# Kernel optimization log

Measured on AMD Instinct MI355X. Metric: run time of the kernel, lower is better.

Reference implementation:

```python
import jax, jax.numpy as jnp
import numpy as np

# NF4 codebook (QLoRA): 16 quantile values of a standard normal, normalized to [-1, 1]
NF4_TABLE = jnp.array([
    -1.0, -0.6961928009986877, -0.5250730514526367, -0.39491748809814453,
    -0.28444138169288635, -0.18477343022823334, -0.09105003625154495, 0.0,
    0.07958029955625534, 0.16093020141124725, 0.24611230194568634,
    0.33791524171829224, 0.44070982933044434, 0.5626170039176941,
    0.7229568362236328, 1.0], dtype=jnp.float32)

IN_DIM = 4096
OUT_DIM = 4096
RANK = 16
ALPHA = 32.0
BLOCK = 64  # NF4 quantization block size along the flattened weight


def setup_inputs() -> dict:
    key = jax.random.key(0)
    k1, k2, k3, k4, k5 = jax.random.split(key, 5)
    x = jax.random.normal(k1, (4, 2048, IN_DIM), dtype=jnp.float32)
    # 4-bit codes into NF4_TABLE, stored unpacked as int32
    w_codes = jax.random.randint(k2, (OUT_DIM, IN_DIM), 0, 16, dtype=jnp.int32)
    # per-block absmax scales (positive)
    w_scales = jax.random.uniform(k3, (OUT_DIM, IN_DIM // BLOCK), dtype=jnp.float32) * 0.02 + 1e-3
    # lora_a: kaiming-uniform-ish scale; lora_b: nonzero for testability (original inits to zeros)
    lora_a = jax.random.normal(k4, (RANK, IN_DIM), dtype=jnp.float32) * (1.0 / np.sqrt(IN_DIM))
    lora_b = jax.random.normal(k5, (OUT_DIM, RANK), dtype=jnp.float32) * 0.01
    return {"x": x, "w_codes": w_codes, "w_scales": w_scales, "lora_a": lora_a, "lora_b": lora_b}


def _dequant_nf4(w_codes, w_scales):
    # codes [O, I] -> dequantized weight [O, I]
    w = NF4_TABLE[w_codes]                                   # [O, I]
    w = w.reshape(OUT_DIM, IN_DIM // BLOCK, BLOCK) * w_scales[:, :, None]
    return w.reshape(OUT_DIM, IN_DIM)


def reference(x, w_codes, w_scales, lora_a, lora_b):
    # base: frozen NF4 linear (dequantize then matmul), no bias
    w = _dequant_nf4(w_codes, w_scales)                      # [O, I]
    base = jnp.einsum('bsi,oi->bso', x, w)                   # [B, S, O]
    # LoRA path: dropout p=0.0 -> identity; scale alpha / rank
    ax = jnp.einsum('bsi,ri->bsr', x, lora_a)                # [B, S, r]
    lora = jnp.einsum('bsr,or->bso', ax, lora_b)             # [B, S, O]
    return base + (ALPHA / RANK) * lora
```

## Files before the change

kernel.cpp:

```cpp
#include <hip/hip_runtime.h>
#include <hip/hip_bf16.h>


#define IN_DIM  4096
#define OUT_DIM 4096
#define RANK    16
#define M_TOK   8192
#define LORA_SCALE 2.0f

typedef __bf16 bf16_t;
typedef bf16_t bf16x8 __attribute__((ext_vector_type(8)));
typedef float  f32x4  __attribute__((ext_vector_type(4)));

__device__ __constant__ float NF4_TAB[16] = {
    -1.0f, -0.6961928009986877f, -0.5250730514526367f, -0.39491748809814453f,
    -0.28444138169288635f, -0.18477343022823334f, -0.09105003625154495f, 0.0f,
    0.07958029955625534f, 0.16093020141124725f, 0.24611230194568634f,
    0.33791524171829224f, 0.44070982933044434f, 0.5626170039176941f,
    0.7229568362236328f, 1.0f};

__global__ __launch_bounds__(256) void prep_w(
    const int* __restrict__ codes, const float* __restrict__ scales,
    const float* __restrict__ la, const float* __restrict__ lb,
    bf16_t* __restrict__ W)
{
    __shared__ float nf4s[16];
    __shared__ float lbs[4][16];
    const int o0 = blockIdx.x * 4;
    const int tid = threadIdx.x;
    if (tid < 64) lbs[tid >> 4][tid & 15] = lb[(o0 + (tid >> 4)) * RANK + (tid & 15)] * LORA_SCALE;
    else if (tid < 80) nf4s[tid - 64] = NF4_TAB[tid - 64];
    __syncthreads();

    #pragma unroll
    for (int it = 0; it < 2; ++it) {
        const int i0 = (it * 256 + tid) * 8;
        float w[4][8];
        #pragma unroll
        for (int oo = 0; oo < 4; ++oo) {
            const size_t base = (size_t)(o0 + oo) * IN_DIM + i0;
            int4 c0 = *(const int4*)(codes + base);
            int4 c1 = *(const int4*)(codes + base + 4);
            const float sc = scales[(o0 + oo) * (IN_DIM / 64) + (i0 >> 6)];
            w[oo][0] = nf4s[c0.x] * sc; w[oo][1] = nf4s[c0.y] * sc;
            w[oo][2] = nf4s[c0.z] * sc; w[oo][3] = nf4s[c0.w] * sc;
            w[oo][4] = nf4s[c1.x] * sc; w[oo][5] = nf4s[c1.y] * sc;
            w[oo][6] = nf4s[c1.z] * sc; w[oo][7] = nf4s[c1.w] * sc;
        }
        #pragma unroll
        for (int r = 0; r < RANK; ++r) {
            float4 a0 = *(const float4*)(la + r * IN_DIM + i0);
            float4 a1 = *(const float4*)(la + r * IN_DIM + i0 + 4);
            #pragma unroll
            for (int oo = 0; oo < 4; ++oo) {
                const float b = lbs[oo][r];
                w[oo][0] += b * a0.x; w[oo][1] += b * a0.y;
                w[oo][2] += b * a0.z; w[oo][3] += b * a0.w;
                w[oo][4] += b * a1.x; w[oo][5] += b * a1.y;
                w[oo][6] += b * a1.z; w[oo][7] += b * a1.w;
            }
        }
        #pragma unroll
        for (int oo = 0; oo < 4; ++oo) {
            bf16x8 v;
            #pragma unroll
            for (int j = 0; j < 8; ++j) v[j] = (bf16_t)w[oo][j];
            *(bf16x8*)(W + (size_t)(o0 + oo) * IN_DIM + i0) = v;
        }
    }
}

__global__ __launch_bounds__(256) void cast_x(
    const float* __restrict__ x, bf16_t* __restrict__ y, int n8)
{
    const int stride = gridDim.x * blockDim.x;
    for (int i = blockIdx.x * blockDim.x + threadIdx.x; i < n8; i += stride) {
        const size_t e = (size_t)i * 8;
        float4 a = *(const float4*)(x + e);
        float4 b = *(const float4*)(x + e + 4);
        bf16x8 v;
        v[0] = (bf16_t)a.x; v[1] = (bf16_t)a.y; v[2] = (bf16_t)a.z; v[3] = (bf16_t)a.w;
        v[4] = (bf16_t)b.x; v[5] = (bf16_t)b.y; v[6] = (bf16_t)b.z; v[7] = (bf16_t)b.w;
        *(bf16x8*)(y + e) = v;
    }
}

__global__ __launch_bounds__(512, 2) void gemm_bt(
    const bf16_t* __restrict__ A, const bf16_t* __restrict__ B,
    float* __restrict__ C)
{
    __shared__ __align__(128) char lds[131072];

    const int tid  = threadIdx.x;
    const int wave = tid >> 6;
    const int lane = tid & 63;

    const int flat = blockIdx.y * gridDim.x + blockIdx.x;
    const int swz  = (flat & 7) * 64 + (flat >> 3);
    const int bx = swz & 15;
    const int by = swz >> 4;
    const int m0 = by * 256;
    const int n0 = bx * 256;

    const int wr = wave >> 2;
    const int wc = wave & 3;

    f32x4 acc[8][4];
    #pragma unroll
    for (int i = 0; i < 8; ++i)
        #pragma unroll
        for (int j = 0; j < 4; ++j) acc[i][j] = (f32x4)0.0f;

    const int frow = lane & 15;
    const int fch  = lane >> 4;

    int offA[8], offB0[2], offB1[2];
    #pragma unroll
    for (int f = 0; f < 8; ++f) {
        const int r = wr * 128 + f * 16 + frow;
        offA[f] = r * 64 + ((fch ^ ((r >> 1) & 3)) << 4);
    }
    #pragma unroll
    for (int n = 0; n < 2; ++n) {
        const int c0 = wc * 64 + n * 16 + frow;
        offB0[n] = c0 * 64 + ((fch ^ ((c0 >> 1) & 3)) << 4);
        const int c1 = wc * 64 + 32 + n * 16 + frow;
        offB1[n] = c1 * 64 + ((fch ^ ((c1 >> 1) & 3)) << 4);
    }

    const int d0 = tid * 16, d1 = 8192 + tid * 16;
    const int sr0 = d0 >> 6, sr1 = d1 >> 6;
    const int sg0 = ((d0 >> 4) & 3) ^ ((sr0 >> 1) & 3);
    const int sg1 = ((d1 >> 4) & 3) ^ ((sr1 >> 1) & 3);
    const char* gA = (const char*)A;
    const char* gB = (const char*)B;

    bf16x8 fA[8], fB0[2], fB1[2];

#define DS_A(SL, KH) do {                                                      \
    const char* bA_ = lds + (SL) * 65536 + (KH) * 16384;                       \
    _Pragma("unroll")                                                          \
    for (int f_ = 0; f_ < 8; ++f_) fA[f_] = *(const bf16x8*)(bA_ + offA[f_]);  \
} while (0)

#define DS_B(SL, KH, FB, OFB) do {                                             \
    const char* bB_ = lds + (SL) * 65536 + 32768 + (KH) * 16384;               \
    FB[0] = *(const bf16x8*)(bB_ + OFB[0]);                                    \
    FB[1] = *(const bf16x8*)(bB_ + OFB[1]);                                    \
} while (0)

#define STG(OPI, KH_, SL, T) do {                                              \
    const char* g_  = (OPI) ? gB : gA;                                         \
    const int   r0_ = (OPI) ? n0 : m0;                                         \
    const size_t ko_ = (size_t)(T) * 128 + (KH_) * 64;                         \
    const char* s0_ = g_ + (size_t)(r0_ + sr0) * 8192 + ko_ + (sg0 << 4);      \
    const char* s1_ = g_ + (size_t)(r0_ + sr1) * 8192 + ko_ + (sg1 << 4);      \
    char* db_ = lds + (SL) * 65536 + (OPI) * 32768 + (KH_) * 16384 + wave * 1024; \
    __builtin_amdgcn_global_load_lds(                                          \
        (const __attribute__((address_space(1))) void*)s0_,                    \
        (__attribute__((address_space(3))) void*)db_, 16, 0, 0);               \
    __builtin_amdgcn_global_load_lds(                                          \
        (const __attribute__((address_space(1))) void*)s1_,                    \
        (__attribute__((address_space(3))) void*)(db_ + 8192), 16, 0, 0);      \
} while (0)

#define MM(NH, FB) do {                                                        \
    __builtin_amdgcn_s_setprio(1);                                             \
    _Pragma("unroll")                                                          \
    for (int f_ = 0; f_ < 8; ++f_) {                                           \
        acc[f_][(NH)*2+0] = __builtin_amdgcn_mfma_f32_16x16x32_bf16(           \
            fA[f_], FB[0], acc[f_][(NH)*2+0], 0, 0, 0);                        \
        acc[f_][(NH)*2+1] = __builtin_amdgcn_mfma_f32_16x16x32_bf16(           \
            fA[f_], FB[1], acc[f_][(NH)*2+1], 0, 0, 0);                        \
    }                                                                          \
    __builtin_amdgcn_s_setprio(0);                                             \
} while (0)

#define BAR __builtin_amdgcn_s_barrier()
#define LG0 do { asm volatile("s_waitcnt lgkmcnt(0)" ::: "memory");            \
                 __builtin_amdgcn_sched_barrier(0); } while (0)
#define VM4 asm volatile("s_waitcnt vmcnt(4)" ::: "memory")
#define VM0 asm volatile("s_waitcnt vmcnt(0)" ::: "memory")

    STG(0, 0, 0, 0); STG(1, 0, 0, 0); STG(0, 1, 0, 0); STG(1, 1, 0, 0);
    STG(0, 0, 1, 1); STG(1, 0, 1, 1);
    VM4;
    BAR;

    for (int i = 0; i < 31; ++i) {
        const int tY  = 2 * i + 1;
        const int tX2 = 2 * i + 2;
        const int tY2 = 2 * i + 3;
        DS_A(0, 0); DS_B(0, 0, fB0, offB0); STG(0, 1, 1, tY);
        BAR; LG0; MM(0, fB0); BAR;
        DS_B(0, 0, fB1, offB1); STG(1, 1, 1, tY);
        BAR; LG0; MM(1, fB1); BAR;
        DS_A(0, 1); DS_B(0, 1, fB0, offB0); STG(0, 0, 0, tX2);
        BAR; LG0; MM(0, fB0); BAR;
        DS_B(0, 1, fB1, offB1); STG(1, 0, 0, tX2);
        VM4; BAR; LG0; MM(1, fB1); BAR;
        DS_A(1, 0); DS_B(1, 0, fB0, offB0); STG(0, 1, 0, tX2);
        BAR; LG0; MM(0, fB0); BAR;
        DS_B(1, 0, fB1, offB1); STG(1, 1, 0, tX2);
        BAR; LG0; MM(1, fB1); BAR;
        DS_A(1, 1); DS_B(1, 1, fB0, offB0); STG(0, 0, 1, tY2);
        BAR; LG0; MM(0, fB0); BAR;
        DS_B(1, 1, fB1, offB1); STG(1, 0, 1, tY2);
        VM4; BAR; LG0; MM(1, fB1); BAR;
    }

    DS_A(0, 0); DS_B(0, 0, fB0, offB0); STG(0, 1, 1, 63);
    BAR; LG0; MM(0, fB0); BAR;
    DS_B(0, 0, fB1, offB1); STG(1, 1, 1, 63);
    BAR; LG0; MM(1, fB1); BAR;
    DS_A(0, 1); DS_B(0, 1, fB0, offB0);
    BAR; LG0; MM(0, fB0); BAR;
    DS_B(0, 1, fB1, offB1);
    VM0; BAR; LG0; MM(1, fB1); BAR;
    DS_A(1, 0); DS_B(1, 0, fB0, offB0);
    BAR; LG0; MM(0, fB0); BAR;
    DS_B(1, 0, fB1, offB1);
    BAR; LG0; MM(1, fB1); BAR;
    DS_A(1, 1); DS_B(1, 1, fB0, offB0);
    BAR; LG0; MM(0, fB0); BAR;
    DS_B(1, 1, fB1, offB1);
    LG0; MM(1, fB1);

    const int crow = (lane >> 4) * 4;
    const int ccol = lane & 15;
    #pragma unroll
    for (int i = 0; i < 8; ++i) {
        #pragma unroll
        for (int j = 0; j < 4; ++j) {
            const int mb = m0 + wr * 128 + i * 16 + crow;
            const int nb = n0 + wc * 64 + j * 16 + ccol;
            #pragma unroll
            for (int r = 0; r < 4; ++r)
                C[(size_t)(mb + r) * OUT_DIM + nb] = acc[i][j][r];
        }
    }
#undef DS_A
#undef DS_B
#undef STG
#undef MM
#undef BAR
#undef LG0
#undef VM4
#undef VM0
}

extern "C" void kernel_launch(void* const* d_in, const int* in_sizes, int n_in,
                              void* d_out, int out_size, void* d_ws, size_t ws_size,
                              hipStream_t stream) {
    const float* x      = (const float*)d_in[0];
    const int*   codes  = (const int*)d_in[1];
    const float* scales = (const float*)d_in[2];
    const float* la     = (const float*)d_in[3];
    const float* lb     = (const float*)d_in[4];
    float* out = (float*)d_out;

    bf16_t* W  = (bf16_t*)d_ws;
    bf16_t* xb = (bf16_t*)((char*)d_ws + (size_t)OUT_DIM * IN_DIM * 2);

    prep_w<<<OUT_DIM / 4, 256, 0, stream>>>(codes, scales, la, lb, W);
    cast_x<<<2048, 256, 0, stream>>>(x, xb, (M_TOK * IN_DIM) / 8);

    dim3 grid(OUT_DIM / 256, M_TOK / 256);
    gemm_bt<<<grid, 512, 0, stream>>>(xb, W, out);
}
```

Measured before the change: 298.3 us.

## Double-buffer LDS fragment registers to overlap reads with MFMA in GEMM loop

Restructures the main GEMM loop into eight phases that prefetch the next A/B fragments from LDS into alternate register sets (even/odd) while the current MFMAs run, removing the per-phase lgkmcnt(0) wait before compute. Offsets are simplified into a single base plus constant strides, and the epilogue is folded into a uniform 32-iteration loop. In the last iteration it issues wrapped-around loads that are never used. The change raises register pressure from the doubled fragment arrays, and relies on compiler-inserted waits for correctness.

```diff
diff --git a/kernel.cpp b/kernel.cpp
--- a/kernel.cpp
+++ b/kernel.cpp
@@ -113,20 +113,9 @@
 
     const int frow = lane & 15;
     const int fch  = lane >> 4;
-
-    int offA[8], offB0[2], offB1[2];
-    #pragma unroll
-    for (int f = 0; f < 8; ++f) {
-        const int r = wr * 128 + f * 16 + frow;
-        offA[f] = r * 64 + ((fch ^ ((r >> 1) & 3)) << 4);
-    }
-    #pragma unroll
-    for (int n = 0; n < 2; ++n) {
-        const int c0 = wc * 64 + n * 16 + frow;
-        offB0[n] = c0 * 64 + ((fch ^ ((c0 >> 1) & 3)) << 4);
-        const int c1 = wc * 64 + 32 + n * 16 + frow;
-        offB1[n] = c1 * 64 + ((fch ^ ((c1 >> 1) & 3)) << 4);
-    }
+    const int fxor = (fch ^ ((frow >> 1) & 3)) << 4;
+    const int aoff = (wr * 128 + frow) * 64 + fxor;
+    const int boff = (wc * 64  + frow) * 64 + fxor;
 
     const int d0 = tid * 16, d1 = 8192 + tid * 16;
     const int sr0 = d0 >> 6, sr1 = d1 >> 6;
@@ -135,21 +124,22 @@
     const char* gA = (const char*)A;
     const char* gB = (const char*)B;
 
-    bf16x8 fA[8], fB0[2], fB1[2];
-
-#define DS_A(SL, KH) do {                                                      \
-    const char* bA_ = lds + (SL) * 65536 + (KH) * 16384;                       \
+    bf16x8 fAe[8], fAo[8], fBe[2], fBo[2];
+
+#define RD_A(FA, SL, KH) do {                                                  \
+    const char* b_ = lds + (SL) * 65536 + (KH) * 16384;                        \
     _Pragma("unroll")                                                          \
-    for (int f_ = 0; f_ < 8; ++f_) fA[f_] = *(const bf16x8*)(bA_ + offA[f_]);  \
-} while (0)
-
-#define DS_B(SL, KH, FB, OFB) do {                                             \
-    const char* bB_ = lds + (SL) * 65536 + 32768 + (KH) * 16384;               \
-    FB[0] = *(const bf16x8*)(bB_ + OFB[0]);                                    \
-    FB[1] = *(const bf16x8*)(bB_ + OFB[1]);                                    \
-} while (0)
-
-#define STG(OPI, KH_, SL, T) do {                                              \
+    for (int f_ = 0; f_ < 8; ++f_)                                             \
+        FA[f_] = *(const bf16x8*)(b_ + aoff + f_ * 1024);                      \
+} while (0)
+
+#define RD_B(FB, SL, KH, NH) do {                                              \
+    const char* b_ = lds + (SL) * 65536 + 32768 + (KH) * 16384;                \
+    FB[0] = *(const bf16x8*)(b_ + boff + (NH) * 2048);                         \
+    FB[1] = *(const bf16x8*)(b_ + boff + (NH) * 2048 + 1024);                  \
+} while (0)
+
+#define STG1(OPI, KH_, SL, T) do {                                             \
     const char* g_  = (OPI) ? gB : gA;                                         \
     const int   r0_ = (OPI) ? n0 : m0;                                         \
     const size_t ko_ = (size_t)(T) * 128 + (KH_) * 64;                         \
@@ -164,67 +154,47 @@
         (__attribute__((address_space(3))) void*)(db_ + 8192), 16, 0, 0);      \
 } while (0)
 
-#define MM(NH, FB) do {                                                        \
+#define MM(FA, FB, NH) do {                                                    \
     __builtin_amdgcn_s_setprio(1);                                             \
     _Pragma("unroll")                                                          \
     for (int f_ = 0; f_ < 8; ++f_) {                                           \
         acc[f_][(NH)*2+0] = __builtin_amdgcn_mfma_f32_16x16x32_bf16(           \
-            fA[f_], FB[0], acc[f_][(NH)*2+0], 0, 0, 0);                        \
+            FA[f_], FB[0], acc[f_][(NH)*2+0], 0, 0, 0);                        \
         acc[f_][(NH)*2+1] = __builtin_amdgcn_mfma_f32_16x16x32_bf16(           \
-            fA[f_], FB[1], acc[f_][(NH)*2+1], 0, 0, 0);                        \
+            FA[f_], FB[1], acc[f_][(NH)*2+1], 0, 0, 0);                        \
     }                                                                          \
     __builtin_amdgcn_s_setprio(0);                                             \
 } while (0)
 
-#define BAR __builtin_amdgcn_s_barrier()
-#define LG0 do { asm volatile("s_waitcnt lgkmcnt(0)" ::: "memory");            \
-                 __builtin_amdgcn_sched_barrier(0); } while (0)
-#define VM4 asm volatile("s_waitcnt vmcnt(4)" ::: "memory")
-#define VM0 asm volatile("s_waitcnt vmcnt(0)" ::: "memory")
-
-    STG(0, 0, 0, 0); STG(1, 0, 0, 0); STG(0, 1, 0, 0); STG(1, 1, 0, 0);
-    STG(0, 0, 1, 1); STG(1, 0, 1, 1);
-    VM4;
-    BAR;
-
-    for (int i = 0; i < 31; ++i) {
-        const int tY  = 2 * i + 1;
-        const int tX2 = 2 * i + 2;
-        const int tY2 = 2 * i + 3;
-        DS_A(0, 0); DS_B(0, 0, fB0, offB0); STG(0, 1, 1, tY);
-        BAR; LG0; MM(0, fB0); BAR;
-        DS_B(0, 0, fB1, offB1); STG(1, 1, 1, tY);
-        BAR; LG0; MM(1, fB1); BAR;
-        DS_A(0, 1); DS_B(0, 1, fB0, offB0); STG(0, 0, 0, tX2);
-        BAR; LG0; MM(0, fB0); BAR;
-        DS_B(0, 1, fB1, offB1); STG(1, 0, 0, tX2);
-        VM4; BAR; LG0; MM(1, fB1); BAR;
-        DS_A(1, 0); DS_B(1, 0, fB0, offB0); STG(0, 1, 0, tX2);
-        BAR; LG0; MM(0, fB0); BAR;
-        DS_B(1, 0, fB1, offB1); STG(1, 1, 0, tX2);
-        BAR; LG0; MM(1, fB1); BAR;
-        DS_A(1, 1); DS_B(1, 1, fB0, offB0); STG(0, 0, 1, tY2);
-        BAR; LG0; MM(0, fB0); BAR;
-        DS_B(1, 1, fB1, offB1); STG(1, 0, 1, tY2);
-        VM4; BAR; LG0; MM(1, fB1); BAR;
-    }
-
-    DS_A(0, 0); DS_B(0, 0, fB0, offB0); STG(0, 1, 1, 63);
-    BAR; LG0; MM(0, fB0); BAR;
-    DS_B(0, 0, fB1, offB1); STG(1, 1, 1, 63);
-    BAR; LG0; MM(1, fB1); BAR;
-    DS_A(0, 1); DS_B(0, 1, fB0, offB0);
-    BAR; LG0; MM(0, fB0); BAR;
-    DS_B(0, 1, fB1, offB1);
-    VM0; BAR; LG0; MM(1, fB1); BAR;
-    DS_A(1, 0); DS_B(1, 0, fB0, offB0);
-    BAR; LG0; MM(0, fB0); BAR;
-    DS_B(1, 0, fB1, offB1);
-    BAR; LG0; MM(1, fB1); BAR;
-    DS_A(1, 1); DS_B(1, 1, fB0, offB0);
-    BAR; LG0; MM(0, fB0); BAR;
-    DS_B(1, 1, fB1, offB1);
-    LG0; MM(1, fB1);
+#define PHASE(SOP, SKH, SSL, ST, CHK, FA, FB, NH, ...) do {                    \
+    __VA_ARGS__;                                                               \
+    STG1(SOP, SKH, SSL, ST);                                                   \
+    if (CHK) { asm volatile("s_waitcnt vmcnt(8)" ::: "memory"); }              \
+    __builtin_amdgcn_sched_barrier(0);                                         \
+    __builtin_amdgcn_s_barrier();                                              \
+    MM(FA, FB, NH);                                                            \
+    __builtin_amdgcn_s_barrier();                                              \
+} while (0)
+
+    STG1(0, 0, 0, 0); STG1(1, 0, 0, 0); STG1(0, 1, 0, 0); STG1(1, 1, 0, 0);
+    STG1(0, 0, 1, 1); STG1(1, 0, 1, 1); STG1(0, 1, 1, 1);
+    asm volatile("s_waitcnt vmcnt(6)" ::: "memory");
+    __builtin_amdgcn_s_barrier();
+    RD_A(fAe, 0, 0); RD_B(fBe, 0, 0, 0);
+
+    for (int i = 0; i < 32; ++i) {
+        const int tS0 = (2 * i + 2) & 63;
+        const int tS1 = (2 * i + 3) & 63;
+        const int tY  = (2 * i + 1) & 63;
+        PHASE(1, 1, 1, tY,  1, fAe, fBe, 0, RD_B(fBo, 0, 0, 1));
+        PHASE(0, 0, 0, tS0, 0, fAe, fBo, 1, RD_A(fAo, 0, 1); RD_B(fBe, 0, 1, 0));
+        PHASE(1, 0, 0, tS0, 1, fAo, fBe, 0, RD_B(fBo, 0, 1, 1));
+        PHASE(0, 1, 0, tS0, 0, fAo, fBo, 1, RD_A(fAe, 1, 0); RD_B(fBe, 1, 0, 0));
+        PHASE(1, 1, 0, tS0, 1, fAe, fBe, 0, RD_B(fBo, 1, 0, 1));
+        PHASE(0, 0, 1, tS1, 0, fAe, fBo, 1, RD_A(fAo, 1, 1); RD_B(fBe, 1, 1, 0));
+        PHASE(1, 0, 1, tS1, 1, fAo, fBe, 0, RD_B(fBo, 1, 1, 1));
+        PHASE(0, 1, 1, tS1, 0, fAo, fBo, 1, RD_A(fAe, 0, 0); RD_B(fBe, 0, 0, 0));
+    }
 
     const int crow = (lane >> 4) * 4;
     const int ccol = lane & 15;
@@ -239,14 +209,11 @@
                 C[(size_t)(mb + r) * OUT_DIM + nb] = acc[i][j][r];
         }
     }
-#undef DS_A
-#undef DS_B
-#undef STG
+#undef RD_A
+#undef RD_B
+#undef STG1
 #undef MM
-#undef BAR
-#undef LG0
-#undef VM4
-#undef VM0
+#undef PHASE
 }
 
 extern "C" void kernel_launch(void* const* d_in, const int* in_sizes, int n_in,
```

Measured after the change: 298.4 us. Within noise of the previous version (+0.0%).
